# Kernel optimization log

Measured on AMD Instinct MI355X. Metric: run time of the kernel, lower is better.

Reference implementation:

```python
import jax, jax.numpy as jnp
import numpy as np

B, Q, NCLS1, C = 8, 900, 11, 256
NUM_ANCHOR = 100
H, W = 200, 200


def _make_view(b):
    # maps homogeneous (x0, y0, x1, y1, 1) box coords (meters-ish) to BEV pixels:
    # pixel = 20 * coord + 100  (keeps random boxes inside the 200x200 grid)
    v = np.zeros((5, 5), dtype=np.float32)
    for i in range(4):
        v[i, i] = 20.0
        v[i, 4] = 100.0
    v[4, 4] = 1.0
    return jnp.asarray(np.broadcast_to(v, (b, 5, 5)).copy())


def setup_inputs() -> dict:
    key = jax.random.key(0)
    k1, k2, k3 = jax.random.split(key, 3)
    return {
        "pred_boxes": jax.random.normal(k1, (B, Q, 4), dtype=jnp.float32),
        "pred_logits": jax.random.normal(k2, (B, Q, NCLS1), dtype=jnp.float32),
        "box_feats": jax.random.normal(k3, (B, Q, C), dtype=jnp.float32),
        "view": _make_view(B),
    }


def _box_to_bev(pred_boxes, pred_logits, box_feats, view):
    # scores = max over non-background classes of softmax(logits)
    scores = jnp.max(jax.nn.softmax(pred_logits, axis=-1)[..., :-1], axis=-1)  # [b,Q]
    _, idx = jax.lax.top_k(scores, NUM_ANCHOR)                                 # [b,N]

    boxes = jnp.take_along_axis(pred_boxes, idx[:, :, None], axis=1)[..., :4]  # [b,N,4]
    feats = jnp.take_along_axis(box_feats, idx[:, :, None], axis=1)            # [b,N,C]

    cx, cy = boxes[..., 0], boxes[..., 1]
    w, h = jnp.exp(boxes[..., 2]), jnp.exp(boxes[..., 3])
    xyxy = jnp.stack([cx - 0.5 * w, cy - 0.5 * h, cx + 0.5 * w, cy + 0.5 * h], axis=-1)
    xyxy1 = jnp.concatenate([xyxy, jnp.ones_like(xyxy[..., :1])], axis=-1)     # [b,N,5]

    coords = jnp.einsum("bij,bnj->bni", view, xyxy1)[..., :4].astype(jnp.int32)
    x0 = jnp.clip(coords[..., 0], 0, W)
    y0 = jnp.clip(coords[..., 1], 0, H)
    x1 = jnp.clip(coords[..., 2], 0, W)
    y1 = jnp.clip(coords[..., 3], 0, H)

    ys = jnp.arange(H, dtype=jnp.int32)
    xs = jnp.arange(W, dtype=jnp.int32)
    row = (ys[None, None, :] >= y0[:, :, None]) & (ys[None, None, :] < y1[:, :, None])  # [b,N,H]
    col = (xs[None, None, :] >= x0[:, :, None]) & (xs[None, None, :] < x1[:, :, None])  # [b,N,W]
    region = row[:, :, :, None] & col[:, :, None, :]                                    # [b,N,H,W]

    bev = jnp.einsum("bnhw,bnc->bhwc", region.astype(feats.dtype), feats)  # [b,H,W,C]
    mask = jnp.any(region, axis=1)                                          # [b,H,W]
    return bev, mask


def reference(pred_boxes, pred_logits, box_feats, view):
    return _box_to_bev(pred_boxes, pred_logits, box_feats, view)
```

## Files before the change

### kernel.cpp

```cpp
#include <hip/hip_runtime.h>
#include <math.h>

#define B_    8
#define Q_    900
#define NCLS_ 11
#define NANC_ 100
#define H_    200
#define W_    200
#define C_    256

__global__ __launch_bounds__(1024) void segdet_topk_kernel(
    const float* __restrict__ pred_boxes,
    const float* __restrict__ pred_logits,
    const float* __restrict__ view,
    int*  __restrict__ ws_idx,
    int4* __restrict__ ws_box)
{
    const int b = blockIdx.x;
    const int q = threadIdx.x;

    __shared__ float sc[Q_];

    if (q < Q_) {
        const float* l = pred_logits + (b * Q_ + q) * NCLS_;
        float v[NCLS_];
        float m = -INFINITY;
        #pragma unroll
        for (int i = 0; i < NCLS_; ++i) { v[i] = l[i]; m = fmaxf(m, v[i]); }
        float s = 0.0f, e10 = -INFINITY;
        #pragma unroll
        for (int i = 0; i < NCLS_; ++i) {
            float e = expf(v[i] - m);
            s += e;
            if (i < NCLS_ - 1) e10 = fmaxf(e10, e);
        }
        sc[q] = e10 / s;
    }
    __syncthreads();

    if (q < Q_) {
        const float my = sc[q];
        int rank = 0;
        for (int j = 0; j < Q_; ++j) {
            float o = sc[j];
            rank += (o > my) || (o == my && j < q);
        }
        if (rank < NANC_) {
            const float* bx = pred_boxes + (b * Q_ + q) * 4;
            double cx = (double)bx[0], cy = (double)bx[1];
            double w  = exp((double)bx[2]);
            double h  = exp((double)bx[3]);
            double p[5] = { cx - 0.5 * w, cy - 0.5 * h,
                            cx + 0.5 * w, cy + 0.5 * h, 1.0 };
            const float* v5 = view + b * 25;
            int ico[4];
            #pragma unroll
            for (int i = 0; i < 4; ++i) {
                double acc = 0.0;
                #pragma unroll
                for (int j = 0; j < 5; ++j) acc += (double)v5[i * 5 + j] * p[j];
                ico[i] = (int)acc;
            }
            int x0 = min(max(ico[0], 0), W_);
            int y0 = min(max(ico[1], 0), H_);
            int x1 = min(max(ico[2], 0), W_);
            int y1 = min(max(ico[3], 0), H_);
            const int slot = b * NANC_ + rank;
            ws_idx[slot] = q;
            ws_box[slot] = make_int4(x0, y0, x1, y1);
        }
    }
}

__global__ __launch_bounds__(256) void segdet_bev_kernel(
    const float* __restrict__ box_feats,
    const int*   __restrict__ ws_idx,
    const int4*  __restrict__ ws_box,
    float* __restrict__ bev,
    float* __restrict__ mask)
{
    const int b = blockIdx.x / H_;
    const int h = blockIdx.x % H_;
    const int c = threadIdx.x;

    __shared__ int s_q[NANC_];
    __shared__ int head_start[W_ + 1];
    __shared__ int head_end[W_ + 1];
    __shared__ int nxt_s[NANC_];
    __shared__ int nxt_e[NANC_];

    if (c <= W_) { head_start[c] = -1; head_end[c] = -1; }
    __syncthreads();

    if (c == 0) {
        int nrow = 0;
        for (int k = 0; k < NANC_; ++k) {
            int4 bxk = ws_box[b * NANC_ + k];
            if (bxk.y <= h && h < bxk.w && bxk.x < bxk.z) {
                int r = nrow++;
                s_q[r] = ws_idx[b * NANC_ + k];
                nxt_s[r] = head_start[bxk.x]; head_start[bxk.x] = r;
                nxt_e[r] = head_end[bxk.z];   head_end[bxk.z]   = r;
            }
        }
    }
    __syncthreads();

    const float* fb = box_feats + (size_t)b * Q_ * C_ + c;
    float* orow = bev + ((size_t)(b * H_ + h) * W_) * C_ + c;
    float* mrow = mask + (size_t)(b * H_ + h) * W_;

    float acc = 0.0f;
    int cnt = 0;
    for (int w = 0; w < W_; ++w) {
        for (int e = head_end[w]; e != -1; e = nxt_e[e]) {
            acc -= fb[s_q[e] * C_];
            --cnt;
        }
        for (int e = head_start[w]; e != -1; e = nxt_s[e]) {
            acc += fb[s_q[e] * C_];
            ++cnt;
        }
        if (cnt == 0) acc = 0.0f;
        orow[(size_t)w * C_] = acc;
        if (c == 0) mrow[w] = (cnt > 0) ? 1.0f : 0.0f;
    }
}

extern "C" void kernel_launch(void* const* d_in, const int* in_sizes, int n_in,
                              void* d_out, int out_size, void* d_ws, size_t ws_size,
                              hipStream_t stream) {
    const float* pred_boxes  = (const float*)d_in[0];
    const float* pred_logits = (const float*)d_in[1];
    const float* box_feats   = (const float*)d_in[2];
    const float* view        = (const float*)d_in[3];

    float* bev  = (float*)d_out;
    float* mask = bev + (size_t)B_ * H_ * W_ * C_;

    int*  ws_idx = (int*)d_ws;
    int4* ws_box = (int4*)((char*)d_ws + 3200);

    segdet_topk_kernel<<<B_, 1024, 0, stream>>>(pred_boxes, pred_logits, view,
                                                ws_idx, ws_box);
    segdet_bev_kernel<<<B_ * H_, 256, 0, stream>>>(box_feats, ws_idx, ws_box,
                                                   bev, mask);
}
```

Before: 123.5 us.

## Replace per-row prefix-sum BEV splat with fp16 MFMA region-times-features GEMM

Replaces the per-row linked-list sweep over box start/end events with a dense GEMM. Each block gathers the top-100 anchor features into LDS as fp16, builds the 0/1 region matrix on the fly from the packed box coordinates, and runs 16x16x32 f16 MFMAs over 128-pixel tiles. Stores become wide float4 writes. The intent is to swap a serial scan with dependent loads for matrix-core throughput and better store coalescing. In exchange, each of the roughly 2500 blocks redoes the feature gather and fp16 conversion, and rounding features to fp16 can lose precision against the fp32 reference.

```diff
diff --git a/kernel.cpp b/kernel.cpp
--- a/kernel.cpp
+++ b/kernel.cpp
@@ -8,6 +8,14 @@
 #define H_    200
 #define W_    200
 #define C_    256
+#define M_    (H_ * W_)
+#define KPAD_ 120
+#define MT_   128
+#define NTILE_ 313
+
+typedef _Float16 half8_ __attribute__((ext_vector_type(8)));
+typedef _Float16 half4_ __attribute__((ext_vector_type(4)));
+typedef float    f32x4_ __attribute__((ext_vector_type(4)));
 
 __global__ __launch_bounds__(1024) void segdet_topk_kernel(
     const float* __restrict__ pred_boxes,
@@ -72,59 +80,91 @@
     }
 }
 
-__global__ __launch_bounds__(256) void segdet_bev_kernel(
+__global__ __launch_bounds__(512, 4) void segdet_gemm_kernel(
     const float* __restrict__ box_feats,
     const int*   __restrict__ ws_idx,
     const int4*  __restrict__ ws_box,
     float* __restrict__ bev,
     float* __restrict__ mask)
 {
-    const int b = blockIdx.x / H_;
-    const int h = blockIdx.x % H_;
-    const int c = threadIdx.x;
+    const int blk = blockIdx.x;
+    const int b   = blk / NTILE_;
+    const int mt  = blk % NTILE_;
+    const int tid = threadIdx.x;
+    const int ln  = tid & 63;
+    const int wv  = tid >> 6;
 
-    __shared__ int s_q[NANC_];
-    __shared__ int head_start[W_ + 1];
-    __shared__ int head_end[W_ + 1];
-    __shared__ int nxt_s[NANC_];
-    __shared__ int nxt_e[NANC_];
+    __shared__ __align__(16) _Float16 sF[C_ * KPAD_ + 64];
+    __shared__ int sB[128];
 
-    if (c <= W_) { head_start[c] = -1; head_end[c] = -1; }
-    __syncthreads();
+    if (tid < 128) {
+        int packed = 0x0000FFFF;
+        if (tid < NANC_) {
+            int4 bx = ws_box[b * NANC_ + tid];
+            packed = bx.x | (bx.y << 8) | (bx.z << 16) | (bx.w << 24);
+        }
+        sB[tid] = packed;
+    }
+    if (tid < 64) sF[C_ * KPAD_ + tid] = (_Float16)0.0f;
 
-    if (c == 0) {
-        int nrow = 0;
-        for (int k = 0; k < NANC_; ++k) {
-            int4 bxk = ws_box[b * NANC_ + k];
-            if (bxk.y <= h && h < bxk.w && bxk.x < bxk.z) {
-                int r = nrow++;
-                s_q[r] = ws_idx[b * NANC_ + k];
-                nxt_s[r] = head_start[bxk.x]; head_start[bxk.x] = r;
-                nxt_e[r] = head_end[bxk.z];   head_end[bxk.z]   = r;
+    for (int it = tid; it < C_ * (KPAD_ / 4); it += 512) {
+        const int kq = it / C_;
+        const int ch = it % C_;
+        half4_ v = { (_Float16)0.0f, (_Float16)0.0f, (_Float16)0.0f, (_Float16)0.0f };
+        if (kq < NANC_ / 4) {
+            #pragma unroll
+            for (int j = 0; j < 4; ++j) {
+                const int k = kq * 4 + j;
+                const int q = ws_idx[b * NANC_ + k];
+                v[j] = (_Float16)box_feats[((size_t)b * Q_ + q) * C_ + ch];
             }
         }
+        *(half4_*)&sF[ch * KPAD_ + kq * 4] = v;
     }
     __syncthreads();
 
-    const float* fb = box_feats + (size_t)b * Q_ * C_ + c;
-    float* orow = bev + ((size_t)(b * H_ + h) * W_) * C_ + c;
-    float* mrow = mask + (size_t)(b * H_ + h) * W_;
+    const int pxbase = mt * MT_ + wv * 16;
+    if (pxbase >= M_) return;
 
-    float acc = 0.0f;
-    int cnt = 0;
-    for (int w = 0; w < W_; ++w) {
-        for (int e = head_end[w]; e != -1; e = nxt_e[e]) {
-            acc -= fb[s_q[e] * C_];
-            --cnt;
+    const int m0 = pxbase + (ln & 15);
+    const int hh = m0 / W_;
+    const int ww = m0 % W_;
+    const int kg = (ln >> 4) * 8;
+
+    f32x4_ acc[16];
+    #pragma unroll
+    for (int i = 0; i < 16; ++i) acc[i] = (f32x4_){0.f, 0.f, 0.f, 0.f};
+    int mor = 0;
+
+    #pragma unroll
+    for (int ks = 0; ks < 4; ++ks) {
+        half8_ rb;
+        #pragma unroll
+        for (int j = 0; j < 8; ++j) {
+            const int k  = ks * 32 + kg + j;
+            const int pk = sB[k];
+            const int x0 = pk & 0xFF, y0 = (pk >> 8) & 0xFF;
+            const int x1 = (pk >> 16) & 0xFF, y1 = (pk >> 24) & 0xFF;
+            const bool cov = (x0 <= ww) & (ww < x1) & (y0 <= hh) & (hh < y1);
+            rb[j] = (_Float16)(cov ? 1.0f : 0.0f);
+            mor |= (int)cov;
         }
-        for (int e = head_start[w]; e != -1; e = nxt_s[e]) {
-            acc += fb[s_q[e] * C_];
-            ++cnt;
+        #pragma unroll
+        for (int ct = 0; ct < 16; ++ct) {
+            const half8_ fa = *(const half8_*)&sF[(ct * 16 + (ln & 15)) * KPAD_
+                                                  + ks * 32 + kg];
+            acc[ct] = __builtin_amdgcn_mfma_f32_16x16x32_f16(fa, rb, acc[ct], 0, 0, 0);
         }
-        if (cnt == 0) acc = 0.0f;
-        orow[(size_t)w * C_] = acc;
-        if (c == 0) mrow[w] = (cnt > 0) ? 1.0f : 0.0f;
     }
+
+    float* orow = bev + ((size_t)b * M_ + m0) * C_ + (ln >> 4) * 4;
+    #pragma unroll
+    for (int ct = 0; ct < 16; ++ct)
+        *(f32x4_*)(orow + ct * 16) = acc[ct];
+
+    mor |= __shfl_xor(mor, 16);
+    mor |= __shfl_xor(mor, 32);
+    if (ln < 16) mask[(size_t)b * M_ + pxbase + ln] = mor ? 1.0f : 0.0f;
 }
 
 extern "C" void kernel_launch(void* const* d_in, const int* in_sizes, int n_in,
@@ -136,13 +176,13 @@
     const float* view        = (const float*)d_in[3];
 
     float* bev  = (float*)d_out;
-    float* mask = bev + (size_t)B_ * H_ * W_ * C_;
+    float* mask = bev + (size_t)B_ * M_ * C_;
 
     int*  ws_idx = (int*)d_ws;
     int4* ws_box = (int4*)((char*)d_ws + 3200);
 
     segdet_topk_kernel<<<B_, 1024, 0, stream>>>(pred_boxes, pred_logits, view,
                                                 ws_idx, ws_box);
-    segdet_bev_kernel<<<B_ * H_, 256, 0, stream>>>(box_feats, ws_idx, ws_box,
-                                                   bev, mask);
+    segdet_gemm_kernel<<<B_ * NTILE_, 512, 0, stream>>>(box_feats, ws_idx, ws_box,
+                                                        bev, mask);
 }
```

Result: slower. 143.2 us (+16.0%).

## Split BEV rows into per-wave width windows with vectorized nontemporal stores

Applied to the files above, without the earlier changes.

The BEV kernel now assigns each wavefront one 25-pixel window of a row instead of one block per full row. Each wave builds its active-box and start/end event lists with ballot compaction, then sorts the events. Each lane handles four channels with float4 loads and nontemporal float4 stores, which should raise parallelism and store efficiency on the large 328 MB output write. The top-k kernel is spread over 8 blocks per batch, each ranking a chunk of queries with float4 shared-memory reads. In exchange, every block recomputes the softmax scores and every window re-sums its initially covered boxes.

```diff
diff --git a/kernel.cpp b/kernel.cpp
--- a/kernel.cpp
+++ b/kernel.cpp
@@ -8,21 +8,28 @@
 #define H_    200
 #define W_    200
 #define C_    256
-
-__global__ __launch_bounds__(1024) void segdet_topk_kernel(
+#define CHNK_ 113
+#define WIN_  25
+#define NWIN_ (W_ / WIN_)
+#define NTASK_ (B_ * H_ * NWIN_)
+
+typedef float f32x4_ __attribute__((ext_vector_type(4)));
+
+__global__ __launch_bounds__(128) void segdet_topk_kernel(
     const float* __restrict__ pred_boxes,
     const float* __restrict__ pred_logits,
     const float* __restrict__ view,
     int*  __restrict__ ws_idx,
     int4* __restrict__ ws_box)
 {
-    const int b = blockIdx.x;
-    const int q = threadIdx.x;
-
-    __shared__ float sc[Q_];
-
-    if (q < Q_) {
-        const float* l = pred_logits + (b * Q_ + q) * NCLS_;
+    const int b     = blockIdx.x >> 3;
+    const int chunk = blockIdx.x & 7;
+    const int tid   = threadIdx.x;
+
+    __shared__ __align__(16) float sc[Q_];
+
+    for (int q2 = tid; q2 < Q_; q2 += 128) {
+        const float* l = pred_logits + (b * Q_ + q2) * NCLS_;
         float v[NCLS_];
         float m = -INFINITY;
         #pragma unroll
@@ -34,16 +41,22 @@
             s += e;
             if (i < NCLS_ - 1) e10 = fmaxf(e10, e);
         }
-        sc[q] = e10 / s;
+        sc[q2] = e10 / s;
     }
     __syncthreads();
 
-    if (q < Q_) {
+    const int q = chunk * CHNK_ + tid;
+    if (tid < CHNK_ && q < Q_) {
         const float my = sc[q];
         int rank = 0;
-        for (int j = 0; j < Q_; ++j) {
-            float o = sc[j];
-            rank += (o > my) || (o == my && j < q);
+        #pragma unroll 4
+        for (int j4 = 0; j4 < Q_ / 4; ++j4) {
+            const float4 o = *(const float4*)&sc[j4 * 4];
+            const int j = j4 * 4;
+            rank += (o.x > my) || (o.x == my && (j + 0) < q);
+            rank += (o.y > my) || (o.y == my && (j + 1) < q);
+            rank += (o.z > my) || (o.z == my && (j + 2) < q);
+            rank += (o.w > my) || (o.w == my && (j + 3) < q);
         }
         if (rank < NANC_) {
             const float* bx = pred_boxes + (b * Q_ + q) * 4;
@@ -72,6 +85,10 @@
     }
 }
 
+__device__ __forceinline__ void nt_store4(float* p, f32x4_ v) {
+    __builtin_nontemporal_store(v, (f32x4_*)p);
+}
+
 __global__ __launch_bounds__(256) void segdet_bev_kernel(
     const float* __restrict__ box_feats,
     const int*   __restrict__ ws_idx,
@@ -79,51 +96,107 @@
     float* __restrict__ bev,
     float* __restrict__ mask)
 {
-    const int b = blockIdx.x / H_;
-    const int h = blockIdx.x % H_;
-    const int c = threadIdx.x;
-
-    __shared__ int s_q[NANC_];
-    __shared__ int head_start[W_ + 1];
-    __shared__ int head_end[W_ + 1];
-    __shared__ int nxt_s[NANC_];
-    __shared__ int nxt_e[NANC_];
-
-    if (c <= W_) { head_start[c] = -1; head_end[c] = -1; }
-    __syncthreads();
-
-    if (c == 0) {
-        int nrow = 0;
-        for (int k = 0; k < NANC_; ++k) {
-            int4 bxk = ws_box[b * NANC_ + k];
-            if (bxk.y <= h && h < bxk.w && bxk.x < bxk.z) {
-                int r = nrow++;
-                s_q[r] = ws_idx[b * NANC_ + k];
-                nxt_s[r] = head_start[bxk.x]; head_start[bxk.x] = r;
-                nxt_e[r] = head_end[bxk.z];   head_end[bxk.z]   = r;
+    const int ln   = threadIdx.x & 63;
+    const int wv   = threadIdx.x >> 6;
+    const int task = blockIdx.x * 4 + wv;
+    if (task >= NTASK_) return;
+
+    const int rid = task / NWIN_;
+    const int jw  = task % NWIN_;
+    const int b   = rid / H_;
+    const int h   = rid % H_;
+    const int w0  = jw * WIN_;
+    const int wlast = w0 + WIN_ - 1;
+
+    __shared__ int s_ini[4][104];
+    __shared__ int s_ev [4][204];
+    __shared__ int s_evs[4][204];
+
+    const unsigned long long lmask = (1ull << ln) - 1ull;
+
+    int nini = 0, nev = 0;
+    #pragma unroll
+    for (int it = 0; it < 2; ++it) {
+        const int k = it * 64 + ln;
+        bool ic = false, oc = false, cc = false;
+        int qi = 0, x0 = 0, x1 = 0;
+        if (k < NANC_) {
+            const int4 bx = ws_box[b * NANC_ + k];
+            qi = ws_idx[b * NANC_ + k];
+            x0 = bx.x; x1 = bx.z;
+            const bool act = (bx.y <= h) && (h < bx.w) && (x0 < x1);
+            ic = act && (x0 <= w0) && (w0 < x1);
+            oc = act && (x0 >  w0) && (x0 <= wlast);
+            cc = act && (x1 >  w0) && (x1 <= wlast);
+        }
+        unsigned long long bi = __ballot(ic);
+        int pos = nini + (int)__popcll(bi & lmask);
+        if (ic) s_ini[wv][pos] = qi;
+        nini += (int)__popcll(bi);
+
+        unsigned long long bo = __ballot(oc);
+        pos = nev + (int)__popcll(bo & lmask);
+        if (oc) s_ev[wv][pos] = qi | (x0 << 10);
+        nev += (int)__popcll(bo);
+
+        unsigned long long bc = __ballot(cc);
+        pos = nev + (int)__popcll(bc & lmask);
+        if (cc) s_ev[wv][pos] = (int)((unsigned)qi | ((unsigned)x1 << 10)
+                                      | 0x80000000u);
+        nev += (int)__popcll(bc);
+    }
+
+    for (int base = 0; base < nev; base += 64) {
+        const int e = base + ln;
+        if (e < nev) {
+            const int me = s_ev[wv][e];
+            const int mypix = (me >> 10) & 0xFF;
+            int rank = 0;
+            for (int j = 0; j < nev; ++j) {
+                const int pj = (s_ev[wv][j] >> 10) & 0xFF;
+                rank += (pj < mypix) || (pj == mypix && j < e);
             }
-        }
-    }
-    __syncthreads();
-
-    const float* fb = box_feats + (size_t)b * Q_ * C_ + c;
-    float* orow = bev + ((size_t)(b * H_ + h) * W_) * C_ + c;
-    float* mrow = mask + (size_t)(b * H_ + h) * W_;
-
-    float acc = 0.0f;
-    int cnt = 0;
-    for (int w = 0; w < W_; ++w) {
-        for (int e = head_end[w]; e != -1; e = nxt_e[e]) {
-            acc -= fb[s_q[e] * C_];
-            --cnt;
-        }
-        for (int e = head_start[w]; e != -1; e = nxt_s[e]) {
-            acc += fb[s_q[e] * C_];
-            ++cnt;
-        }
-        if (cnt == 0) acc = 0.0f;
-        orow[(size_t)w * C_] = acc;
-        if (c == 0) mrow[w] = (cnt > 0) ? 1.0f : 0.0f;
+            s_evs[wv][rank] = me;
+        }
+    }
+
+    const float* fbase = box_feats + (size_t)b * Q_ * C_ + ln * 4;
+    f32x4_ acc = {0.f, 0.f, 0.f, 0.f};
+    int cnt = nini;
+    int i = 0;
+    for (; i + 4 <= nini; i += 4) {
+        const int q0 = s_ini[wv][i + 0];
+        const int q1 = s_ini[wv][i + 1];
+        const int q2 = s_ini[wv][i + 2];
+        const int q3 = s_ini[wv][i + 3];
+        const f32x4_ a0 = *(const f32x4_*)(fbase + (size_t)q0 * C_);
+        const f32x4_ a1 = *(const f32x4_*)(fbase + (size_t)q1 * C_);
+        const f32x4_ a2 = *(const f32x4_*)(fbase + (size_t)q2 * C_);
+        const f32x4_ a3 = *(const f32x4_*)(fbase + (size_t)q3 * C_);
+        acc += a0; acc += a1; acc += a2; acc += a3;
+    }
+    for (; i < nini; ++i) {
+        const int q0 = s_ini[wv][i];
+        acc += *(const f32x4_*)(fbase + (size_t)q0 * C_);
+    }
+
+    float* obase = bev + ((size_t)rid * W_ + w0) * C_ + ln * 4;
+    float* mrow  = mask + (size_t)rid * W_ + w0;
+
+    int p = 0;
+    for (int d = 0; d < WIN_; ++d) {
+        const int w = w0 + d;
+        while (p < nev && ((s_evs[wv][p] >> 10) & 0xFF) == w) {
+            const int ent = s_evs[wv][p];
+            const f32x4_ f = *(const f32x4_*)(fbase + (size_t)(ent & 0x3FF) * C_);
+            if (ent < 0) { acc -= f; --cnt; }
+            else         { acc += f; ++cnt; }
+            ++p;
+        }
+        if (cnt == 0) acc = (f32x4_){0.f, 0.f, 0.f, 0.f};
+        nt_store4(obase + (size_t)d * C_, acc);
+        if (ln == 0) __builtin_nontemporal_store((cnt > 0) ? 1.0f : 0.0f,
+                                                 &mrow[d]);
     }
 }
 
@@ -141,8 +214,8 @@
     int*  ws_idx = (int*)d_ws;
     int4* ws_box = (int4*)((char*)d_ws + 3200);
 
-    segdet_topk_kernel<<<B_, 1024, 0, stream>>>(pred_boxes, pred_logits, view,
-                                                ws_idx, ws_box);
-    segdet_bev_kernel<<<B_ * H_, 256, 0, stream>>>(box_feats, ws_idx, ws_box,
-                                                   bev, mask);
-}
+    segdet_topk_kernel<<<B_ * 8, 128, 0, stream>>>(pred_boxes, pred_logits, view,
+                                                   ws_idx, ws_box);
+    segdet_bev_kernel<<<NTASK_ / 4, 256, 0, stream>>>(box_feats, ws_idx, ws_box,
+                                                      bev, mask);
+}
```

New measurement: 126.9 us. 2.8% more time.
